# Performance work log

Measured on AMD Instinct MI355X. Metric: run time of the kernel, lower is better.

Reference implementation:

```python
import jax, jax.numpy as jnp
import numpy as np

N_NODES = 100000


def _gcn_norm(edge_index, num_nodes):
    # PyG gcn_norm with add_self_loops=True, symmetric normalization.
    src = jnp.concatenate([edge_index[0], jnp.arange(num_nodes)])
    dst = jnp.concatenate([edge_index[1], jnp.arange(num_nodes)])
    ones = jnp.ones(src.shape[0], dtype=jnp.float32)
    deg = jax.ops.segment_sum(ones, dst, num_segments=num_nodes)
    dinv = jnp.where(deg > 0, jax.lax.rsqrt(deg), 0.0)
    norm = dinv[src] * dinv[dst]  # [E + N]
    return src, dst, norm


def _gcn_conv(x, W, b, src, dst, norm, num_nodes):
    h = x @ W                                  # dense transform first (PyG order)
    msg = h[src] * norm[:, None]               # gather + scale, [E+N, D]
    agg = jax.ops.segment_sum(msg, dst, num_segments=num_nodes)
    return agg + b


def setup_inputs() -> dict:
    key = jax.random.key(0)
    ks = jax.random.split(key, 6)
    F_in, D, C, E = 256, 64, 47, 1200000
    x = jax.random.normal(ks[0], (N_NODES, F_in), dtype=jnp.float32)
    edge_index = jax.random.randint(ks[1], (2, E), 0, N_NODES)
    W1 = jax.random.normal(ks[2], (F_in, D), dtype=jnp.float32) * (1.0 / np.sqrt(F_in))
    b1 = jnp.zeros((D,), dtype=jnp.float32)
    W2 = jax.random.normal(ks[3], (D, C), dtype=jnp.float32) * (1.0 / np.sqrt(D))
    b2 = jnp.zeros((C,), dtype=jnp.float32)
    return {"x": x, "edge_index": edge_index, "W1": W1, "b1": b1, "W2": W2, "b2": b2}


def reference(x, edge_index, W1, b1, W2, b2):
    src, dst, norm = _gcn_norm(edge_index, N_NODES)
    h = jax.nn.relu(_gcn_conv(x, W1, b1, src, dst, norm, N_NODES))
    # dropout: eval mode (training=False) -> identity
    out = _gcn_conv(h, W2, b2, src, dst, norm, N_NODES)
    return jax.nn.log_softmax(out, axis=1)
```

## Files before the change

### kernel.cpp

```cpp
#include <hip/hip_runtime.h>
#include <math.h>

#define NN 100000
#define FIN 256
#define D1 64
#define C2 47
#define S2 48
#define PREPB 76
#define NBKT 1563
#define CAP 1024
#define EPB 4096

typedef unsigned short u16;
typedef unsigned int u32;
typedef __attribute__((ext_vector_type(8))) short short8;
typedef __attribute__((ext_vector_type(4))) float floatx4;

__device__ __forceinline__ u16 f2b(float f) {
    union { float f; unsigned u; } v; v.f = f;
    unsigned r = v.u + 0x7FFF + ((v.u >> 16) & 1);
    return (u16)(r >> 16);
}
__device__ __forceinline__ float b2f_lo(u32 p) { union { unsigned u; float f; } v; v.u = p << 16; return v.f; }
__device__ __forceinline__ float b2f_hi(u32 p) { union { unsigned u; float f; } v; v.u = p & 0xFFFF0000u; return v.f; }

__global__ __launch_bounds__(256) void k_prep_bucket(
    const float* __restrict__ W1, const float* __restrict__ W2,
    u16* __restrict__ W1t, u16* __restrict__ W2t,
    const int* __restrict__ src, const int* __restrict__ dst, int E,
    int* __restrict__ bucketCnt, u32* __restrict__ ebuf)
{
    int b = blockIdx.x;
    if (b < PREPB) {
        int i = b * 256 + threadIdx.x;
        if (i < FIN * D1) {
            int c = i >> 8, k = i & 255;
            W1t[i] = f2b(W1[k * D1 + c]);
        } else if (i < FIN * D1 + D1 * S2) {
            int j = i - FIN * D1;
            int c = j >> 6, k = j & 63;
            W2t[j] = (c < C2) ? f2b(W2[k * C2 + c]) : (u16)0;
        }
        return;
    }
    __shared__ int hist[NBKT];
    __shared__ int base[NBKT];
    const int t = threadIdx.x;
    const int blk = b - PREPB;
    for (int i = t; i < NBKT; i += 256) hist[i] = 0;
    __syncthreads();

    int e0 = blk * EPB + t;
    u32 pk[16]; int bk[16], tk[16];
    #pragma unroll
    for (int j = 0; j < 16; ++j) {
        int e = e0 + j * 256;
        bk[j] = -1;
        if (e < E) {
            int d = dst[e];
            bk[j] = d >> 6;
            pk[j] = (u32)src[e] | ((u32)(d & 63) << 17);
            tk[j] = atomicAdd(&hist[bk[j]], 1);
        }
    }
    __syncthreads();
    for (int i = t; i < NBKT; i += 256)
        base[i] = hist[i] ? atomicAdd(&bucketCnt[i], hist[i]) : 0;
    __syncthreads();
    #pragma unroll
    for (int j = 0; j < 16; ++j)
        if (bk[j] >= 0) {
            int pos = base[bk[j]] + tk[j];
            if (pos < CAP) ebuf[(size_t)bk[j] * CAP + pos] = pk[j];
        }
}

__global__ __launch_bounds__(256) void k_gemm1(
    const int* __restrict__ bucketCnt, const u32* __restrict__ ebuf,
    const float* __restrict__ x, const u16* __restrict__ W1t,
    float* __restrict__ dinv, u16* __restrict__ hs1)
{
    __shared__ short As[2][64 * 40];
    __shared__ short Bs[2][64 * 40];
    __shared__ int hist[64];
    __shared__ float dinvs[64];
    const int b = blockIdx.x;
    const int t = threadIdx.x;
    const int bm = b * 64;

    if (t < 64) hist[t] = 0;
    __syncthreads();
    {
        int cnt = bucketCnt[b]; if (cnt > CAP) cnt = CAP;
        const u32* eb = ebuf + (size_t)b * CAP;
        for (int i = t; i < cnt; i += 256)
            atomicAdd(&hist[(eb[i] >> 17) & 63], 1);
    }
    __syncthreads();
    if (t < 64) {
        float dv = rsqrtf((float)hist[t] + 1.0f);
        dinvs[t] = dv;
        dinv[bm + t] = dv;
    }

    const int w = t >> 6, lane = t & 63;
    const int arow = t >> 2;
    const int ak0 = (t & 3) * 8;

    floatx4 acc[4] = {};
    const int gr = bm + arow;
    const bool rowok = gr < NN;
    const float* xrow = x + (size_t)(rowok ? gr : 0) * FIN + ak0;

    float4 v0 = make_float4(0.f,0.f,0.f,0.f), v1 = v0;
    if (rowok) { v0 = *(const float4*)(xrow); v1 = *(const float4*)(xrow + 4); }
    short8 wv = *(const short8*)(W1t + arow * FIN + ak0);
    {
        short8 av;
        av[0]=(short)f2b(v0.x); av[1]=(short)f2b(v0.y); av[2]=(short)f2b(v0.z); av[3]=(short)f2b(v0.w);
        av[4]=(short)f2b(v1.x); av[5]=(short)f2b(v1.y); av[6]=(short)f2b(v1.z); av[7]=(short)f2b(v1.w);
        *(short8*)(&As[0][arow * 40 + ak0]) = av;
        *(short8*)(&Bs[0][arow * 40 + ak0]) = wv;
    }
    __syncthreads();

    int cb_ = 0;
    for (int kt = 32; kt <= FIN; kt += 32) {
        const bool more = kt < FIN;
        float4 n0, n1; short8 nw;
        if (more) {
            if (rowok) { n0 = *(const float4*)(xrow + kt); n1 = *(const float4*)(xrow + kt + 4); }
            else { n0 = make_float4(0.f,0.f,0.f,0.f); n1 = n0; }
            nw = *(const short8*)(W1t + arow * FIN + kt + ak0);
        }
        short8 af = *(const short8*)(&As[cb_][(w * 16 + (lane & 15)) * 40 + (lane >> 4) * 8]);
        #pragma unroll
        for (int cb = 0; cb < 4; ++cb) {
            short8 bv = *(const short8*)(&Bs[cb_][(cb * 16 + (lane & 15)) * 40 + (lane >> 4) * 8]);
            acc[cb] = __builtin_amdgcn_mfma_f32_16x16x32_bf16(af, bv, acc[cb], 0, 0, 0);
        }
        if (!more) break;
        short8 av;
        av[0]=(short)f2b(n0.x); av[1]=(short)f2b(n0.y); av[2]=(short)f2b(n0.z); av[3]=(short)f2b(n0.w);
        av[4]=(short)f2b(n1.x); av[5]=(short)f2b(n1.y); av[6]=(short)f2b(n1.z); av[7]=(short)f2b(n1.w);
        *(short8*)(&As[cb_ ^ 1][arow * 40 + ak0]) = av;
        *(short8*)(&Bs[cb_ ^ 1][arow * 40 + ak0]) = nw;
        __syncthreads();
        cb_ ^= 1;
    }

    #pragma unroll
    for (int cb = 0; cb < 4; ++cb) {
        #pragma unroll
        for (int r = 0; r < 4; ++r) {
            int rl = w * 16 + (lane >> 4) * 4 + r;
            int grow = bm + rl;
            if (grow < NN) {
                float v = acc[cb][r] * dinvs[rl];
                hs1[(size_t)grow * D1 + cb * 16 + (lane & 15)] = f2b(v);
            }
        }
    }
}

__device__ __forceinline__ void bucket_sort_lds(
    const u32* __restrict__ eb, int cnt, int t,
    u32* elds, u32* sorted, int* hist, int* rp, int* cur)
{
    if (t < 64) hist[t] = 0;
    __syncthreads();
    for (int i = t; i < cnt; i += 256) {
        u32 p = eb[i];
        elds[i] = p;
        atomicAdd(&hist[(p >> 17) & 63], 1);
    }
    __syncthreads();
    if (t < 64) {
        int h = hist[t];
        int v = h;
        #pragma unroll
        for (int off = 1; off < 64; off <<= 1) {
            int u = __shfl_up(v, off);
            if (t >= off) v += u;
        }
        rp[t + 1] = v;
        cur[t] = v - h;
        if (t == 0) rp[0] = 0;
    }
    __syncthreads();
    for (int i = t; i < cnt; i += 256) {
        u32 p = elds[i];
        int pos = atomicAdd(&cur[(p >> 17) & 63], 1);
        sorted[pos] = p & 0x1FFFF;
    }
    __syncthreads();
}

__global__ __launch_bounds__(256) void k_gather_gemm2(
    const int* __restrict__ bucketCnt, const u32* __restrict__ ebuf,
    const float* __restrict__ dinv, const u16* __restrict__ hs1,
    const float* __restrict__ b1, const u16* __restrict__ W2t,
    u16* __restrict__ hs2)
{
    __shared__ u32 elds[CAP];
    __shared__ u32 sorted[CAP];
    __shared__ int hist[64], rp[65], cur[64];
    __shared__ short As[2][64 * 40];
    __shared__ short Bs[2][48 * 40];
    __shared__ float dinvs[64];
    __shared__ float b1s[64];
    const int t = threadIdx.x;
    const int b = blockIdx.x, bm = b * 64;
    const int w = t >> 6, lane = t & 63;
    const int g = t >> 3, l8 = t & 7;

    for (int s = t; s < 384; s += 256) {
        int kt = s / 192, rem = s - kt * 192;
        int r = rem >> 2, j = rem & 3;
        *(short8*)(&Bs[kt][r * 40 + j * 8]) =
            *(const short8*)(W2t + r * D1 + kt * 32 + j * 8);
    }
    if (t < 64) { dinvs[t] = dinv[bm + t]; b1s[t] = b1[t]; }

    int cnt = bucketCnt[b]; if (cnt > CAP) cnt = CAP;
    bucket_sort_lds(ebuf + (size_t)b * CAP, cnt, t, elds, sorted, hist, rp, cur);

    {
        const int col = 8 * l8;
        const int kth = l8 >> 2;
        const int cs  = col & 31;
        float4 bbl = *(const float4*)(b1s + col);
        float4 bbh = *(const float4*)(b1s + col + 4);
        #pragma unroll 1
        for (int i = 0; i < 2; ++i) {
            int rl = g * 2 + i;
            int node = bm + rl;
            if (node >= NN) break;
            int beg = rp[rl], end = rp[rl + 1];
            uint4 sp = *((const uint4*)(hs1 + (size_t)node * D1) + l8);
            float a0=b2f_lo(sp.x), a1=b2f_hi(sp.x), a2=b2f_lo(sp.y), a3=b2f_hi(sp.y);
            float a4=b2f_lo(sp.z), a5=b2f_hi(sp.z), a6=b2f_lo(sp.w), a7=b2f_hi(sp.w);
            float c0=0.f,c1=0.f,c2=0.f,c3=0.f,c4=0.f,c5=0.f,c6=0.f,c7=0.f;
            int e = beg;
            for (; e + 4 <= end; e += 4) {
                int s0 = sorted[e+0], s1 = sorted[e+1], s2 = sorted[e+2], s3 = sorted[e+3];
                uint4 p0 = *((const uint4*)(hs1 + (size_t)s0 * D1) + l8);
                uint4 p1 = *((const uint4*)(hs1 + (size_t)s1 * D1) + l8);
                uint4 p2 = *((const uint4*)(hs1 + (size_t)s2 * D1) + l8);
                uint4 p3 = *((const uint4*)(hs1 + (size_t)s3 * D1) + l8);
                a0+=b2f_lo(p0.x); a1+=b2f_hi(p0.x); a2+=b2f_lo(p0.y); a3+=b2f_hi(p0.y);
                a4+=b2f_lo(p0.z); a5+=b2f_hi(p0.z); a6+=b2f_lo(p0.w); a7+=b2f_hi(p0.w);
                c0+=b2f_lo(p1.x); c1+=b2f_hi(p1.x); c2+=b2f_lo(p1.y); c3+=b2f_hi(p1.y);
                c4+=b2f_lo(p1.z); c5+=b2f_hi(p1.z); c6+=b2f_lo(p1.w); c7+=b2f_hi(p1.w);
                a0+=b2f_lo(p2.x); a1+=b2f_hi(p2.x); a2+=b2f_lo(p2.y); a3+=b2f_hi(p2.y);
                a4+=b2f_lo(p2.z); a5+=b2f_hi(p2.z); a6+=b2f_lo(p2.w); a7+=b2f_hi(p2.w);
                c0+=b2f_lo(p3.x); c1+=b2f_hi(p3.x); c2+=b2f_lo(p3.y); c3+=b2f_hi(p3.y);
                c4+=b2f_lo(p3.z); c5+=b2f_hi(p3.z); c6+=b2f_lo(p3.w); c7+=b2f_hi(p3.w);
            }
            for (; e < end; ++e) {
                uint4 p0 = *((const uint4*)(hs1 + (size_t)sorted[e] * D1) + l8);
                a0+=b2f_lo(p0.x); a1+=b2f_hi(p0.x); a2+=b2f_lo(p0.y); a3+=b2f_hi(p0.y);
                a4+=b2f_lo(p0.z); a5+=b2f_hi(p0.z); a6+=b2f_lo(p0.w); a7+=b2f_hi(p0.w);
            }
            float dd = dinvs[rl];
            float r0 = fmaxf(fmaf(dd, a0 + c0, bbl.x), 0.f);
            float r1 = fmaxf(fmaf(dd, a1 + c1, bbl.y), 0.f);
            float r2 = fmaxf(fmaf(dd, a2 + c2, bbl.z), 0.f);
            float r3 = fmaxf(fmaf(dd, a3 + c3, bbl.w), 0.f);
            float r4 = fmaxf(fmaf(dd, a4 + c4, bbh.x), 0.f);
            float r5 = fmaxf(fmaf(dd, a5 + c5, bbh.y), 0.f);
            float r6 = fmaxf(fmaf(dd, a6 + c6, bbh.z), 0.f);
            float r7 = fmaxf(fmaf(dd, a7 + c7, bbh.w), 0.f);
            short8 pk;
            pk[0]=(short)f2b(r0); pk[1]=(short)f2b(r1); pk[2]=(short)f2b(r2); pk[3]=(short)f2b(r3);
            pk[4]=(short)f2b(r4); pk[5]=(short)f2b(r5); pk[6]=(short)f2b(r6); pk[7]=(short)f2b(r7);
            *(short8*)(&As[kth][rl * 40 + cs]) = pk;
        }
    }
    __syncthreads();

    floatx4 acc2[3] = {};
    #pragma unroll
    for (int kt = 0; kt < 2; ++kt) {
        short8 af = *(const short8*)(&As[kt][(w * 16 + (lane & 15)) * 40 + (lane >> 4) * 8]);
        #pragma unroll
        for (int cb = 0; cb < 3; ++cb) {
            short8 bv = *(const short8*)(&Bs[kt][(cb * 16 + (lane & 15)) * 40 + (lane >> 4) * 8]);
            acc2[cb] = __builtin_amdgcn_mfma_f32_16x16x32_bf16(af, bv, acc2[cb], 0, 0, 0);
        }
    }

    #pragma unroll
    for (int cb = 0; cb < 3; ++cb) {
        #pragma unroll
        for (int r = 0; r < 4; ++r) {
            int rl2 = w * 16 + (lane >> 4) * 4 + r;
            int grow = bm + rl2;
            if (grow < NN) {
                float v = acc2[cb][r] * dinvs[rl2];
                hs2[(size_t)grow * S2 + cb * 16 + (lane & 15)] = f2b(v);
            }
        }
    }
}

__global__ __launch_bounds__(256) void k_gather47(
    const int* __restrict__ bucketCnt, const u32* __restrict__ ebuf,
    const float* __restrict__ dinv, const u16* __restrict__ hs2,
    const float* __restrict__ b2, float* __restrict__ out)
{
    __shared__ u32 elds[CAP];
    __shared__ u32 sorted[CAP];
    __shared__ int hist[64], rp[65], cur[64];
    __shared__ float dinvs[64];
    __shared__ float b2s[48];
    const int t = threadIdx.x;
    const int b = blockIdx.x, bm = b * 64;
    const int g = t >> 3, l8 = t & 7;

    if (t < 64) dinvs[t] = dinv[bm + t];
    if (t < 48) b2s[t] = (t < C2) ? b2[t] : 0.f;

    int cnt = bucketCnt[b]; if (cnt > CAP) cnt = CAP;
    bucket_sort_lds(ebuf + (size_t)b * CAP, cnt, t, elds, sorted, hist, rp, cur);

    const bool act = l8 < 6;
    const int lc = act ? l8 : 0;
    #pragma unroll 1
    for (int i = 0; i < 2; ++i) {
        int rl = g * 2 + i;
        int node = bm + rl;
        if (node >= NN) break;
        int beg = rp[rl], end = rp[rl + 1];
        uint4 sp = *((const uint4*)(hs2 + (size_t)node * S2) + lc);
        float a0=b2f_lo(sp.x), a1=b2f_hi(sp.x), a2=b2f_lo(sp.y), a3=b2f_hi(sp.y);
        float a4=b2f_lo(sp.z), a5=b2f_hi(sp.z), a6=b2f_lo(sp.w), a7=b2f_hi(sp.w);
        float c0=0.f,c1=0.f,c2=0.f,c3=0.f,c4=0.f,c5=0.f,c6=0.f,c7=0.f;
        int e = beg;
        for (; e + 4 <= end; e += 4) {
            int s0 = sorted[e+0], s1 = sorted[e+1], s2 = sorted[e+2], s3 = sorted[e+3];
            uint4 p0 = *((const uint4*)(hs2 + (size_t)s0 * S2) + lc);
            uint4 p1 = *((const uint4*)(hs2 + (size_t)s1 * S2) + lc);
            uint4 p2 = *((const uint4*)(hs2 + (size_t)s2 * S2) + lc);
            uint4 p3 = *((const uint4*)(hs2 + (size_t)s3 * S2) + lc);
            a0+=b2f_lo(p0.x); a1+=b2f_hi(p0.x); a2+=b2f_lo(p0.y); a3+=b2f_hi(p0.y);
            a4+=b2f_lo(p0.z); a5+=b2f_hi(p0.z); a6+=b2f_lo(p0.w); a7+=b2f_hi(p0.w);
            c0+=b2f_lo(p1.x); c1+=b2f_hi(p1.x); c2+=b2f_lo(p1.y); c3+=b2f_hi(p1.y);
            c4+=b2f_lo(p1.z); c5+=b2f_hi(p1.z); c6+=b2f_lo(p1.w); c7+=b2f_hi(p1.w);
            a0+=b2f_lo(p2.x); a1+=b2f_hi(p2.x); a2+=b2f_lo(p2.y); a3+=b2f_hi(p2.y);
            a4+=b2f_lo(p2.z); a5+=b2f_hi(p2.z); a6+=b2f_lo(p2.w); a7+=b2f_hi(p2.w);
            c0+=b2f_lo(p3.x); c1+=b2f_hi(p3.x); c2+=b2f_lo(p3.y); c3+=b2f_hi(p3.y);
            c4+=b2f_lo(p3.z); c5+=b2f_hi(p3.z); c6+=b2f_lo(p3.w); c7+=b2f_hi(p3.w);
        }
        for (; e < end; ++e) {
            uint4 p0 = *((const uint4*)(hs2 + (size_t)sorted[e] * S2) + lc);
            a0+=b2f_lo(p0.x); a1+=b2f_hi(p0.x); a2+=b2f_lo(p0.y); a3+=b2f_hi(p0.y);
            a4+=b2f_lo(p0.z); a5+=b2f_hi(p0.z); a6+=b2f_lo(p0.w); a7+=b2f_hi(p0.w);
        }
        float dd = dinvs[rl];
        float fv[8] = { a0+c0, a1+c1, a2+c2, a3+c3, a4+c4, a5+c5, a6+c6, a7+c7 };
        const int fb = 8 * lc;
        float val[8];
        float m = -INFINITY;
        #pragma unroll
        for (int k = 0; k < 8; ++k) {
            int fe = fb + k;
            bool valid = act && (fe < C2);
            val[k] = valid ? fmaf(dd, fv[k], b2s[valid ? fe : 0]) : -INFINITY;
            m = fmaxf(m, val[k]);
        }
        #pragma unroll
        for (int off = 1; off < 8; off <<= 1) m = fmaxf(m, __shfl_xor(m, off));
        float ex = 0.f;
        #pragma unroll
        for (int k = 0; k < 8; ++k)
            if (val[k] > -INFINITY) ex += expf(val[k] - m);
        #pragma unroll
        for (int off = 1; off < 8; off <<= 1) ex += __shfl_xor(ex, off);
        float ls = m + logf(ex);
        #pragma unroll
        for (int k = 0; k < 8; ++k) {
            int fe = fb + k;
            if (act && fe < C2) out[(size_t)node * C2 + fe] = val[k] - ls;
        }
    }
}

extern "C" void kernel_launch(void* const* d_in, const int* in_sizes, int n_in,
                              void* d_out, int out_size, void* d_ws, size_t ws_size,
                              hipStream_t stream) {
    const float* x  = (const float*)d_in[0];
    const int*   ei = (const int*)d_in[1];
    const float* W1 = (const float*)d_in[2];
    const float* b1 = (const float*)d_in[3];
    const float* W2 = (const float*)d_in[4];
    const float* b2 = (const float*)d_in[5];
    float* out = (float*)d_out;

    const int E = in_sizes[1] / 2;
    const int* src = ei;
    const int* dst = ei + E;

    char* ws = (char*)d_ws;
    float* dinv      = (float*)(ws);
    int*   bucketCnt = (int*)(ws + 0x80000);
    u16*   W1t       = (u16*)(ws + 0x180000);
    u16*   W2t       = (u16*)(ws + 0x189000);
    u32*   ebuf      = (u32*)(ws + 0x200000);
    u16*   hs1       = (u16*)(ws + 0xE00000);
    u16*   hs2       = (u16*)(ws + 0x1B00000);

    const int nBk1 = (E + EPB - 1) / EPB;

    hipMemsetAsync(bucketCnt, 0, NBKT * sizeof(int), stream);
    k_prep_bucket<<<PREPB + nBk1, 256, 0, stream>>>(W1, W2, W1t, W2t, src, dst, E,
                                                    bucketCnt, ebuf);
    k_gemm1<<<NBKT, 256, 0, stream>>>(bucketCnt, ebuf, x, W1t, dinv, hs1);
    k_gather_gemm2<<<NBKT, 256, 0, stream>>>(bucketCnt, ebuf, dinv, hs1, b1, W2t, hs2);
    k_gather47<<<NBKT, 256, 0, stream>>>(bucketCnt, ebuf, dinv, hs2, b2, out);
}
```

Measured before the change: 124.3 us.

## Sort bucket edges once in gemm1 and reuse the CSR in both gathers

The per-bucket counting sort of edges by destination now runs once in k_gemm1, which already builds the histogram, and writes the row pointers and sorted source indices to global workspace. The two gather kernels load this precomputed CSR into LDS instead of each repeating the histogram, scan and scatter with LDS atomics. This drops two redundant sorts and their extra barriers, and lowers LDS use in the gather kernels. In exchange it adds global writes and reads of the sorted arrays and a scatter-sort phase inside the gemm kernel.

```diff
diff --git a/kernel.cpp b/kernel.cpp
--- a/kernel.cpp
+++ b/kernel.cpp
@@ -78,11 +78,12 @@
 __global__ __launch_bounds__(256) void k_gemm1(
     const int* __restrict__ bucketCnt, const u32* __restrict__ ebuf,
     const float* __restrict__ x, const u16* __restrict__ W1t,
-    float* __restrict__ dinv, u16* __restrict__ hs1)
+    float* __restrict__ dinv, int* __restrict__ rpg, u32* __restrict__ sortedg,
+    u16* __restrict__ hs1)
 {
     __shared__ short As[2][64 * 40];
     __shared__ short Bs[2][64 * 40];
-    __shared__ int hist[64];
+    __shared__ int hist[64], cur[64];
     __shared__ float dinvs[64];
     const int b = blockIdx.x;
     const int t = threadIdx.x;
@@ -90,17 +91,30 @@
 
     if (t < 64) hist[t] = 0;
     __syncthreads();
-    {
-        int cnt = bucketCnt[b]; if (cnt > CAP) cnt = CAP;
-        const u32* eb = ebuf + (size_t)b * CAP;
-        for (int i = t; i < cnt; i += 256)
-            atomicAdd(&hist[(eb[i] >> 17) & 63], 1);
-    }
+    int cnt = bucketCnt[b]; if (cnt > CAP) cnt = CAP;
+    const u32* eb = ebuf + (size_t)b * CAP;
+    for (int i = t; i < cnt; i += 256)
+        atomicAdd(&hist[(eb[i] >> 17) & 63], 1);
     __syncthreads();
     if (t < 64) {
-        float dv = rsqrtf((float)hist[t] + 1.0f);
+        int h = hist[t];
+        int v = h;
+        #pragma unroll
+        for (int off = 1; off < 64; off <<= 1) {
+            int u = __shfl_up(v, off);
+            if (t >= off) v += u;
+        }
+        cur[t] = v - h;
+        rpg[(size_t)b * 64 + t] = v - h;
+        float dv = rsqrtf((float)h + 1.0f);
         dinvs[t] = dv;
         dinv[bm + t] = dv;
+    }
+    __syncthreads();
+    for (int i = t; i < cnt; i += 256) {
+        u32 p = eb[i];
+        int pos = atomicAdd(&cur[(p >> 17) & 63], 1);
+        sortedg[(size_t)b * CAP + pos] = p & 0x1FFFF;
     }
 
     const int w = t >> 6, lane = t & 63;
@@ -163,48 +177,15 @@
     }
 }
 
-__device__ __forceinline__ void bucket_sort_lds(
-    const u32* __restrict__ eb, int cnt, int t,
-    u32* elds, u32* sorted, int* hist, int* rp, int* cur)
-{
-    if (t < 64) hist[t] = 0;
-    __syncthreads();
-    for (int i = t; i < cnt; i += 256) {
-        u32 p = eb[i];
-        elds[i] = p;
-        atomicAdd(&hist[(p >> 17) & 63], 1);
-    }
-    __syncthreads();
-    if (t < 64) {
-        int h = hist[t];
-        int v = h;
-        #pragma unroll
-        for (int off = 1; off < 64; off <<= 1) {
-            int u = __shfl_up(v, off);
-            if (t >= off) v += u;
-        }
-        rp[t + 1] = v;
-        cur[t] = v - h;
-        if (t == 0) rp[0] = 0;
-    }
-    __syncthreads();
-    for (int i = t; i < cnt; i += 256) {
-        u32 p = elds[i];
-        int pos = atomicAdd(&cur[(p >> 17) & 63], 1);
-        sorted[pos] = p & 0x1FFFF;
-    }
-    __syncthreads();
-}
-
 __global__ __launch_bounds__(256) void k_gather_gemm2(
-    const int* __restrict__ bucketCnt, const u32* __restrict__ ebuf,
+    const int* __restrict__ bucketCnt, const int* __restrict__ rpg,
+    const u32* __restrict__ sortedg,
     const float* __restrict__ dinv, const u16* __restrict__ hs1,
     const float* __restrict__ b1, const u16* __restrict__ W2t,
     u16* __restrict__ hs2)
 {
-    __shared__ u32 elds[CAP];
     __shared__ u32 sorted[CAP];
-    __shared__ int hist[64], rp[65], cur[64];
+    __shared__ int rp[65];
     __shared__ short As[2][64 * 40];
     __shared__ short Bs[2][48 * 40];
     __shared__ float dinvs[64];
@@ -220,10 +201,12 @@
         *(short8*)(&Bs[kt][r * 40 + j * 8]) =
             *(const short8*)(W2t + r * D1 + kt * 32 + j * 8);
     }
-    if (t < 64) { dinvs[t] = dinv[bm + t]; b1s[t] = b1[t]; }
-
     int cnt = bucketCnt[b]; if (cnt > CAP) cnt = CAP;
-    bucket_sort_lds(ebuf + (size_t)b * CAP, cnt, t, elds, sorted, hist, rp, cur);
+    if (t < 64) { dinvs[t] = dinv[bm + t]; b1s[t] = b1[t]; rp[t] = rpg[(size_t)b * 64 + t]; }
+    if (t == 0) rp[64] = cnt;
+    for (int i = t; i < cnt; i += 256)
+        sorted[i] = sortedg[(size_t)b * CAP + i];
+    __syncthreads();
 
     {
         const int col = 8 * l8;
@@ -305,24 +288,26 @@
 }
 
 __global__ __launch_bounds__(256) void k_gather47(
-    const int* __restrict__ bucketCnt, const u32* __restrict__ ebuf,
+    const int* __restrict__ bucketCnt, const int* __restrict__ rpg,
+    const u32* __restrict__ sortedg,
     const float* __restrict__ dinv, const u16* __restrict__ hs2,
     const float* __restrict__ b2, float* __restrict__ out)
 {
-    __shared__ u32 elds[CAP];
     __shared__ u32 sorted[CAP];
-    __shared__ int hist[64], rp[65], cur[64];
+    __shared__ int rp[65];
     __shared__ float dinvs[64];
     __shared__ float b2s[48];
     const int t = threadIdx.x;
     const int b = blockIdx.x, bm = b * 64;
     const int g = t >> 3, l8 = t & 7;
 
-    if (t < 64) dinvs[t] = dinv[bm + t];
+    int cnt = bucketCnt[b]; if (cnt > CAP) cnt = CAP;
+    if (t < 64) { dinvs[t] = dinv[bm + t]; rp[t] = rpg[(size_t)b * 64 + t]; }
     if (t < 48) b2s[t] = (t < C2) ? b2[t] : 0.f;
-
-    int cnt = bucketCnt[b]; if (cnt > CAP) cnt = CAP;
-    bucket_sort_lds(ebuf + (size_t)b * CAP, cnt, t, elds, sorted, hist, rp, cur);
+    if (t == 0) rp[64] = cnt;
+    for (int i = t; i < cnt; i += 256)
+        sorted[i] = sortedg[(size_t)b * CAP + i];
+    __syncthreads();
 
     const bool act = l8 < 6;
     const int lc = act ? l8 : 0;
@@ -406,16 +391,18 @@
     int*   bucketCnt = (int*)(ws + 0x80000);
     u16*   W1t       = (u16*)(ws + 0x180000);
     u16*   W2t       = (u16*)(ws + 0x189000);
+    int*   rpg       = (int*)(ws + 0x190000);
     u32*   ebuf      = (u32*)(ws + 0x200000);
-    u16*   hs1       = (u16*)(ws + 0xE00000);
-    u16*   hs2       = (u16*)(ws + 0x1B00000);
+    u32*   sortedg   = (u32*)(ws + 0x900000);
+    u16*   hs1       = (u16*)(ws + 0x1000000);
+    u16*   hs2       = (u16*)(ws + 0x1E00000);
 
     const int nBk1 = (E + EPB - 1) / EPB;
 
     hipMemsetAsync(bucketCnt, 0, NBKT * sizeof(int), stream);
     k_prep_bucket<<<PREPB + nBk1, 256, 0, stream>>>(W1, W2, W1t, W2t, src, dst, E,
                                                     bucketCnt, ebuf);
-    k_gemm1<<<NBKT, 256, 0, stream>>>(bucketCnt, ebuf, x, W1t, dinv, hs1);
-    k_gather_gemm2<<<NBKT, 256, 0, stream>>>(bucketCnt, ebuf, dinv, hs1, b1, W2t, hs2);
-    k_gather47<<<NBKT, 256, 0, stream>>>(bucketCnt, ebuf, dinv, hs2, b2, out);
-}
+    k_gemm1<<<NBKT, 256, 0, stream>>>(bucketCnt, ebuf, x, W1t, dinv, rpg, sortedg, hs1);
+    k_gather_gemm2<<<NBKT, 256, 0, stream>>>(bucketCnt, rpg, sortedg, dinv, hs1, b1, W2t, hs2);
+    k_gather47<<<NBKT, 256, 0, stream>>>(bucketCnt, rpg, sortedg, dinv, hs2, b2, out);
+}
```

After: 124.3 us. Within noise of the previous version (+0.0%).
